# Kernel tuning notes

Hardware: AMD Instinct MI355X
Metric: run time of the kernel (lower is better)

Reference implementation:

```python
import jax, jax.numpy as jnp
import numpy as np

# 5-tap binomial kernel, same as torch module
_H5 = jnp.array([0.0625, 0.25, 0.375, 0.25, 0.0625], dtype=jnp.float32)
_K1 = _H5[:, None] * _H5[None, :]        # 5x5 Gaussian, sums to 1 (reduce kernel)
_K4 = 4.0 * _K1                           # expand kernel (gain 4)
# polyphase sub-kernels for expand (match torch strided slicing of kernel)
_KER00 = _K4[0::2, 0::2]  # 3x3
_KER01 = _K4[0::2, 1::2]  # 3x2
_KER10 = _K4[1::2, 0::2]  # 2x3
_KER11 = _K4[1::2, 1::2]  # 2x2


def _dwconv(x, k, stride=1):
    """Depthwise valid conv, same kernel per channel. x: NCHW, k: (kh, kw)."""
    C = x.shape[1]
    kern = jnp.broadcast_to(k[None, None].astype(x.dtype), (C, 1) + k.shape)
    return jax.lax.conv_general_dilated(
        x, kern, (stride, stride), 'VALID',
        dimension_numbers=('NCHW', 'OIHW', 'NCHW'),
        feature_group_count=C)


def pyr_reduce(im):
    # replicate-pad 2 each side, 5x5 conv, subsample [0::2,0::2] == stride-2 conv
    x = jnp.pad(im, ((0, 0), (0, 0), (2, 2), (2, 2)), mode='edge')
    return _dwconv(x, _K1, stride=2)


def pyr_expand(im):
    B, C, H, W = im.shape
    x_r2c2 = jnp.pad(im, ((0, 0), (0, 0), (1, 1), (1, 1)), mode='edge')  # top+bot, left+right
    x_r2c1 = jnp.pad(im, ((0, 0), (0, 0), (1, 1), (0, 1)), mode='edge')  # top+bot, right
    x_c2r1 = jnp.pad(im, ((0, 0), (0, 0), (0, 1), (1, 1)), mode='edge')  # bot, left+right
    x_c1r1 = jnp.pad(im, ((0, 0), (0, 0), (0, 1), (0, 1)), mode='edge')  # bot, right
    o00 = _dwconv(x_r2c2, _KER00)  # -> out[0::2, 0::2]
    o01 = _dwconv(x_r2c1, _KER01)  # -> out[0::2, 1::2]
    o10 = _dwconv(x_c2r1, _KER10)  # -> out[1::2, 0::2]
    o11 = _dwconv(x_c1r1, _KER11)  # -> out[1::2, 1::2]
    out = jnp.zeros((B, C, 2 * H, 2 * W), im.dtype)
    out = out.at[:, :, 0::2, 0::2].set(o00)
    out = out.at[:, :, 0::2, 1::2].set(o01)
    out = out.at[:, :, 1::2, 0::2].set(o10)
    out = out.at[:, :, 1::2, 1::2].set(o11)
    return out


def setup_inputs() -> dict:
    key = jax.random.key(0)
    im = jax.random.normal(key, (16, 3, 1024, 1024), dtype=jnp.float32)
    return {"im": im, "levels": 5}


def reference(im, levels):
    gpyr = [im]
    for _ in range(levels - 1):
        gpyr.append(pyr_reduce(gpyr[-1]))
    lpyr = [gpyr[l] - pyr_expand(gpyr[l + 1]) for l in range(levels - 1)]
    lpyr.append(gpyr[-1])
    return tuple(lpyr)
```

## Files before the change

### kernel.cpp

```cpp
#include <hip/hip_runtime.h>


#define RTX 64
#define RTY 4
#define LDSW 132

__launch_bounds__(256)
__global__ void reduce_kernel(const float* __restrict__ in, float* __restrict__ out,
                              int Hin, int Win, int Hout, int Wout) {
    __shared__ float tile[12 * LDSW];
    const int tx = threadIdx.x, ty = threadIdx.y;
    const int p = blockIdx.z;
    const float* src = in + (size_t)p * Hin * Win;

    const int row0 = 2 * (blockIdx.y * RTY) - 2;
    const int col0 = 2 * (blockIdx.x * RTX) - 2;

#pragma unroll
    for (int r = ty; r < 12; r += RTY) {
        int gr = row0 + r;
        gr = gr < 0 ? 0 : (gr >= Hin ? Hin - 1 : gr);
        const float* srow = src + (size_t)gr * Win;
#pragma unroll
        for (int c = tx; c < LDSW; c += RTX) {
            int gc = col0 + c;
            gc = gc < 0 ? 0 : (gc >= Win ? Win - 1 : gc);
            tile[r * LDSW + c] = srow[gc];
        }
    }
    __syncthreads();

    const int j = blockIdx.x * RTX + tx;
    const int i = blockIdx.y * RTY + ty;
    if (i >= Hout || j >= Wout) return;

    const float w0 = 0.0625f, w1 = 0.25f, w2 = 0.375f;
    const float* trow = tile + (2 * ty) * LDSW + 2 * tx;
    float acc = 0.f;
    const float wr[5] = {w0, w1, w2, w1, w0};
#pragma unroll
    for (int a = 0; a < 5; ++a) {
        const float* rr = trow + a * LDSW;
        float s = w0 * rr[0];
        s = fmaf(w1, rr[1], s);
        s = fmaf(w2, rr[2], s);
        s = fmaf(w1, rr[3], s);
        s = fmaf(w0, rr[4], s);
        acc = fmaf(wr[a], s, acc);
    }
    out[(size_t)p * Hout * Wout + (size_t)i * Wout + j] = acc;
}

__launch_bounds__(256)
__global__ void lap_kernel(const float* __restrict__ fine, const float* __restrict__ coarse,
                           float* __restrict__ out, int Hc, int Wc) {
    const int t = blockIdx.x * blockDim.x + threadIdx.x;
    const int i = blockIdx.y * blockDim.y + threadIdx.y;
    const int p = blockIdx.z;
    const int Wc2 = Wc >> 1;
    if (i >= Hc || t >= Wc2) return;

    const float* g = coarse + (size_t)p * Hc * Wc;
    const int im1 = i > 0 ? i - 1 : 0;
    const int ip1 = i < Hc - 1 ? i + 1 : Hc - 1;
    const float* rm = g + (size_t)im1 * Wc;
    const float* r0 = g + (size_t)i   * Wc;
    const float* rp = g + (size_t)ip1 * Wc;

    const int jl = 2 * t - 1 > 0 ? 2 * t - 1 : 0;
    const int jr = 2 * t + 2 < Wc - 1 ? 2 * t + 2 : Wc - 1;

    float cm[4], c0[4], cp[4];
    {
        float2 m = *(const float2*)(rm + 2 * t);
        float2 z = *(const float2*)(r0 + 2 * t);
        float2 q = *(const float2*)(rp + 2 * t);
        cm[1] = m.x; cm[2] = m.y;
        c0[1] = z.x; c0[2] = z.y;
        cp[1] = q.x; cp[2] = q.y;
        cm[0] = rm[jl]; cm[3] = rm[jr];
        c0[0] = r0[jl]; c0[3] = r0[jr];
        cp[0] = rp[jl]; cp[3] = rp[jr];
    }

    float e[4], o[4];
#pragma unroll
    for (int c = 0; c < 4; ++c) {
        e[c] = fmaf(0.125f, cm[c], fmaf(0.75f, c0[c], 0.125f * cp[c]));
        o[c] = 0.5f * (c0[c] + cp[c]);
    }

    float ev0 = fmaf(0.125f, e[0], fmaf(0.75f, e[1], 0.125f * e[2]));
    float ev1 = 0.5f * (e[1] + e[2]);
    float ev2 = fmaf(0.125f, e[1], fmaf(0.75f, e[2], 0.125f * e[3]));
    float ev3 = 0.5f * (e[2] + e[3]);
    float od0 = fmaf(0.125f, o[0], fmaf(0.75f, o[1], 0.125f * o[2]));
    float od1 = 0.5f * (o[1] + o[2]);
    float od2 = fmaf(0.125f, o[1], fmaf(0.75f, o[2], 0.125f * o[3]));
    float od3 = 0.5f * (o[2] + o[3]);

    const int Wf = 2 * Wc;
    const size_t fbase = (size_t)p * (size_t)(2 * Hc) * Wf;
    const float4* f0 = (const float4*)(fine + fbase + (size_t)(2 * i) * Wf);
    const float4* f1 = (const float4*)(fine + fbase + (size_t)(2 * i + 1) * Wf);
    float4 a = f0[t], b = f1[t];

    float4* w0p = (float4*)(out + fbase + (size_t)(2 * i) * Wf);
    float4* w1p = (float4*)(out + fbase + (size_t)(2 * i + 1) * Wf);
    w0p[t] = make_float4(a.x - ev0, a.y - ev1, a.z - ev2, a.w - ev3);
    w1p[t] = make_float4(b.x - od0, b.y - od1, b.z - od2, b.w - od3);
}

extern "C" void kernel_launch(void* const* d_in, const int* in_sizes, int n_in,
                              void* d_out, int out_size, void* d_ws, size_t ws_size,
                              hipStream_t stream) {
    (void)in_sizes; (void)n_in; (void)d_ws; (void)ws_size; (void)out_size;
    const float* im = (const float*)d_in[0];
    float* out = (float*)d_out;

    const int P = 48;
    const int H0 = 1024, W0 = 1024;

    size_t off[5];
    size_t acc = 0;
    for (int l = 0; l < 5; ++l) {
        off[l] = acc;
        int h = H0 >> l, w = W0 >> l;
        acc += (size_t)P * h * w;
    }

    for (int l = 0; l < 4; ++l) {
        int Hin = H0 >> l, Win = W0 >> l;
        int Hout = Hin >> 1, Wout = Win >> 1;
        const float* src = (l == 0) ? im : (out + off[l]);
        float* dst = out + off[l + 1];
        dim3 blk(RTX, RTY, 1);
        dim3 grid((Wout + RTX - 1) / RTX, (Hout + RTY - 1) / RTY, P);
        reduce_kernel<<<grid, blk, 0, stream>>>(src, dst, Hin, Win, Hout, Wout);
    }

    for (int l = 0; l < 4; ++l) {
        int Hc = H0 >> (l + 1), Wc = W0 >> (l + 1);
        const float* fine = (l == 0) ? im : (out + off[l]);
        const float* coarse = out + off[l + 1];
        float* dst = out + off[l];
        dim3 blk(64, 4, 1);
        dim3 grid((Wc / 2 + 63) / 64, (Hc + 3) / 4, P);
        lap_kernel<<<grid, blk, 0, stream>>>(fine, coarse, dst, Hc, Wc);
    }
}
```

Baseline: 578.3 us.

## Register-block reduce kernel with 4x4 outputs per thread and float4 loads

Replaces the LDS-tiled one-output-per-thread reduce with a kernel where each thread computes a 4x4 output block directly from global memory. It uses a separable horizontal-then-vertical filter and vectorized float4 loads, with a template split between interior and edge paths. This removes shared memory staging and barriers and cuts per-output arithmetic. In exchange each thread re-reads overlapping halo rows and columns, relying on caches, and register pressure rises.

Result: faster. 507.7 us (-12.2%).

```diff
diff --git a/kernel.cpp b/kernel.cpp
--- a/kernel.cpp
+++ b/kernel.cpp
@@ -1,54 +1,89 @@
 #include <hip/hip_runtime.h>
 
 
-#define RTX 64
-#define RTY 4
-#define LDSW 132
+#define RBX 64
+#define RBY 4
+
+template <bool EDGE>
+__device__ __forceinline__ void reduce_accum(const float* __restrict__ src,
+                                             int Hin, int Win, int rbase, int cb,
+                                             float (&acc)[4][4]) {
+    const float w0 = 0.0625f, w1 = 0.25f, w2 = 0.375f;
+    const float wr[5] = {w0, w1, w2, w1, w0};
+#pragma unroll
+    for (int rr = 0; rr < 11; ++rr) {
+        int gr = rbase + rr;
+        gr = gr < 0 ? 0 : (gr > Hin - 1 ? Hin - 1 : gr);
+        const float* row = src + (size_t)gr * Win;
+        float v[16];
+        if (!EDGE) {
+#pragma unroll
+            for (int q = 0; q < 4; ++q) {
+                float4 f = *reinterpret_cast<const float4*>(row + cb + 4 * q);
+                v[4 * q + 0] = f.x; v[4 * q + 1] = f.y;
+                v[4 * q + 2] = f.z; v[4 * q + 3] = f.w;
+            }
+        } else {
+#pragma unroll
+            for (int c = 0; c < 16; ++c) {
+                int gc = cb + c;
+                gc = gc < 0 ? 0 : (gc > Win - 1 ? Win - 1 : gc);
+                v[c] = row[gc];
+            }
+        }
+        float h[4];
+#pragma unroll
+        for (int c = 0; c < 4; ++c) {
+            const float* vv = v + 2 + 2 * c;
+            float s04 = vv[0] + vv[4];
+            float s13 = vv[1] + vv[3];
+            float hh = w0 * s04;
+            hh = fmaf(w1, s13, hh);
+            hh = fmaf(w2, vv[2], hh);
+            h[c] = hh;
+        }
+#pragma unroll
+        for (int i = 0; i < 4; ++i) {
+            const int a = rr - 2 * i;
+            if (a >= 0 && a <= 4) {
+                const float w = wr[a];
+#pragma unroll
+                for (int c = 0; c < 4; ++c)
+                    acc[i][c] = fmaf(w, h[c], acc[i][c]);
+            }
+        }
+    }
+}
 
 __launch_bounds__(256)
 __global__ void reduce_kernel(const float* __restrict__ in, float* __restrict__ out,
                               int Hin, int Win, int Hout, int Wout) {
-    __shared__ float tile[12 * LDSW];
-    const int tx = threadIdx.x, ty = threadIdx.y;
     const int p = blockIdx.z;
+    const int t = blockIdx.x * RBX + threadIdx.x;
+    const int i0 = (blockIdx.y * RBY + threadIdx.y) * 4;
+    const int j0 = 4 * t;
+    if (j0 >= Wout || i0 >= Hout) return;
+
     const float* src = in + (size_t)p * Hin * Win;
+    const int cb = 8 * t - 4;
+    const int rbase = 2 * i0 - 2;
+    const bool edge = (cb < 0) | (cb + 15 > Win - 1);
 
-    const int row0 = 2 * (blockIdx.y * RTY) - 2;
-    const int col0 = 2 * (blockIdx.x * RTX) - 2;
+    float acc[4][4];
+#pragma unroll
+    for (int i = 0; i < 4; ++i)
+#pragma unroll
+        for (int c = 0; c < 4; ++c) acc[i][c] = 0.f;
 
+    if (!edge) reduce_accum<false>(src, Hin, Win, rbase, cb, acc);
+    else       reduce_accum<true>(src, Hin, Win, rbase, cb, acc);
+
+    float* drow = out + (size_t)p * Hout * Wout + j0;
 #pragma unroll
-    for (int r = ty; r < 12; r += RTY) {
-        int gr = row0 + r;
-        gr = gr < 0 ? 0 : (gr >= Hin ? Hin - 1 : gr);
-        const float* srow = src + (size_t)gr * Win;
-#pragma unroll
-        for (int c = tx; c < LDSW; c += RTX) {
-            int gc = col0 + c;
-            gc = gc < 0 ? 0 : (gc >= Win ? Win - 1 : gc);
-            tile[r * LDSW + c] = srow[gc];
-        }
+    for (int i = 0; i < 4; ++i) {
+        *reinterpret_cast<float4*>(drow + (size_t)(i0 + i) * Wout) =
+            make_float4(acc[i][0], acc[i][1], acc[i][2], acc[i][3]);
     }
-    __syncthreads();
-
-    const int j = blockIdx.x * RTX + tx;
-    const int i = blockIdx.y * RTY + ty;
-    if (i >= Hout || j >= Wout) return;
-
-    const float w0 = 0.0625f, w1 = 0.25f, w2 = 0.375f;
-    const float* trow = tile + (2 * ty) * LDSW + 2 * tx;
-    float acc = 0.f;
-    const float wr[5] = {w0, w1, w2, w1, w0};
-#pragma unroll
-    for (int a = 0; a < 5; ++a) {
-        const float* rr = trow + a * LDSW;
-        float s = w0 * rr[0];
-        s = fmaf(w1, rr[1], s);
-        s = fmaf(w2, rr[2], s);
-        s = fmaf(w1, rr[3], s);
-        s = fmaf(w0, rr[4], s);
-        acc = fmaf(wr[a], s, acc);
-    }
-    out[(size_t)p * Hout * Wout + (size_t)i * Wout + j] = acc;
 }
 
 __launch_bounds__(256)
@@ -134,8 +169,8 @@
         int Hout = Hin >> 1, Wout = Win >> 1;
         const float* src = (l == 0) ? im : (out + off[l]);
         float* dst = out + off[l + 1];
-        dim3 blk(RTX, RTY, 1);
-        dim3 grid((Wout + RTX - 1) / RTX, (Hout + RTY - 1) / RTY, P);
+        dim3 blk(RBX, RBY, 1);
+        dim3 grid((Wout + 4 * RBX - 1) / (4 * RBX), (Hout + 4 * RBY - 1) / (4 * RBY), P);
         reduce_kernel<<<grid, blk, 0, stream>>>(src, dst, Hin, Win, Hout, Wout);
     }
 
```
